# Performance work log

Hardware: AMD Instinct MI355X
Metric: run time of the kernel (lower is better)

## Reference

```python
import jax, jax.numpy as jnp
import numpy as np

D_MODEL, D_STATE, EXPAND, D_CONV = 96, 16, 2, 3
D_INNER = EXPAND * D_MODEL  # 192
DT_RANK = -(-D_MODEL // 16)  # 6
K = 4
B, H, W = 4, 64, 64


def setup_inputs() -> dict:
    key = jax.random.key(0)
    ks = jax.random.split(key, 12)
    x = jax.random.normal(ks[0], (B, H, W, D_MODEL), jnp.float32)
    in_proj_w = jax.random.normal(ks[1], (2 * D_INNER, D_MODEL), jnp.float32) * 0.02
    conv_w = jax.random.normal(ks[2], (D_INNER, 1, D_CONV, D_CONV), jnp.float32) * 0.1
    conv_b = jnp.zeros((D_INNER,), jnp.float32)
    x_proj_w = jax.random.normal(ks[3], (K, DT_RANK + 2 * D_STATE, D_INNER), jnp.float32) * 0.02
    dt_proj_w = jax.random.uniform(ks[4], (K, D_INNER, DT_RANK), jnp.float32,
                                   -DT_RANK ** -0.5, DT_RANK ** -0.5)
    dt = jnp.exp(jax.random.uniform(ks[5], (K, D_INNER)) *
                 (np.log(0.1) - np.log(0.001)) + np.log(0.001))
    dt = jnp.clip(dt, 1e-4, None)
    dt_proj_b = dt + jnp.log(-jnp.expm1(-dt))  # inverse-softplus init
    A_logs = jnp.tile(jnp.log(jnp.arange(1, D_STATE + 1, dtype=jnp.float32))[None, :],
                      (K * D_INNER, 1))
    Ds = jnp.ones((K * D_INNER,), jnp.float32)
    norm_g = jnp.ones((D_INNER,), jnp.float32)
    norm_b = jnp.zeros((D_INNER,), jnp.float32)
    out_proj_w = jax.random.normal(ks[6], (D_MODEL, D_INNER), jnp.float32) * 0.02
    return dict(x=x, in_proj_w=in_proj_w, conv_w=conv_w, conv_b=conv_b,
                x_proj_w=x_proj_w, dt_proj_w=dt_proj_w, dt_proj_b=dt_proj_b,
                A_logs=A_logs, Ds=Ds, norm_g=norm_g, norm_b=norm_b,
                out_proj_w=out_proj_w)


def _selective_scan(u, delta, A, Bmat, Cmat, Dvec):
    # u,delta: (B,K,D,L)  A: (K,D,N)  Bmat,Cmat: (B,K,N,L)  Dvec: (K,D)
    uT = jnp.moveaxis(u, -1, 0)      # (L,B,K,D)
    dT = jnp.moveaxis(delta, -1, 0)  # (L,B,K,D)
    BT = jnp.moveaxis(Bmat, -1, 0)   # (L,B,K,N)
    CT = jnp.moveaxis(Cmat, -1, 0)   # (L,B,K,N)
    h0 = jnp.zeros(u.shape[:3] + (A.shape[-1],), u.dtype)  # (B,K,D,N)

    def step(h, inp):
        u_t, d_t, B_t, C_t = inp
        dA = jnp.exp(d_t[..., None] * A)                       # (B,K,D,N)
        dBu = (d_t * u_t)[..., None] * B_t[..., None, :]       # (B,K,D,N)
        h = dA * h + dBu
        y = jnp.sum(h * C_t[..., None, :], axis=-1)            # (B,K,D)
        return h, y

    _, ys = jax.lax.scan(step, h0, (uT, dT, BT, CT))
    y = jnp.moveaxis(ys, 0, -1)  # (B,K,D,L)
    return y + Dvec[None, :, :, None] * u


def reference(x, in_proj_w, conv_w, conv_b, x_proj_w, dt_proj_w, dt_proj_b,
              A_logs, Ds, norm_g, norm_b, out_proj_w):
    Bn, Hn, Wn, _ = x.shape
    L = Hn * Wn
    xz = x @ in_proj_w.T                       # (B,H,W,2*Dinner)
    xi, z = jnp.split(xz, 2, axis=-1)
    xi = jnp.transpose(xi, (0, 3, 1, 2))       # (B,Dinner,H,W)
    xi = jax.lax.conv_general_dilated(xi, conv_w, (1, 1), 'SAME',
                                      feature_group_count=D_INNER,
                                      dimension_numbers=('NCHW', 'OIHW', 'NCHW'))
    xi = xi + conv_b[None, :, None, None]
    xi = jax.nn.silu(xi)

    # 4 scan directions
    x_hw = xi.reshape(Bn, D_INNER, L)
    x_wh = jnp.transpose(xi, (0, 1, 3, 2)).reshape(Bn, D_INNER, L)
    x_hwwh = jnp.stack([x_hw, x_wh], axis=1)               # (B,2,D,L)
    xs = jnp.concatenate([x_hwwh, jnp.flip(x_hwwh, axis=-1)], axis=1)  # (B,4,D,L)

    x_dbl = jnp.einsum('bkdl,kcd->bkcl', xs, x_proj_w)
    dts, Bs, Cs = jnp.split(x_dbl, [DT_RANK, DT_RANK + D_STATE], axis=2)
    dts = jnp.einsum('bkrl,kdr->bkdl', dts, dt_proj_w)
    delta = jax.nn.softplus(dts + dt_proj_b[None, :, :, None])

    A = -jnp.exp(A_logs).reshape(K, D_INNER, D_STATE)
    Dv = Ds.reshape(K, D_INNER)
    out_y = _selective_scan(xs, delta, A, Bs, Cs, Dv)       # (B,4,D,L)

    inv_y = jnp.flip(out_y[:, 2:4], axis=-1)                # (B,2,D,L)
    wh_y = jnp.transpose(out_y[:, 1].reshape(Bn, D_INNER, Wn, Hn),
                         (0, 1, 3, 2)).reshape(Bn, D_INNER, L)
    invwh_y = jnp.transpose(inv_y[:, 1].reshape(Bn, D_INNER, Wn, Hn),
                            (0, 1, 3, 2)).reshape(Bn, D_INNER, L)
    y = out_y[:, 0] + inv_y[:, 0] + wh_y + invwh_y          # (B,D,L)

    y = jnp.transpose(y, (0, 2, 1)).reshape(Bn, Hn, Wn, D_INNER)
    mu = jnp.mean(y, axis=-1, keepdims=True)
    var = jnp.var(y, axis=-1, keepdims=True)
    y = (y - mu) * jax.lax.rsqrt(var + 1e-5) * norm_g + norm_b
    y = y * jax.nn.silu(z)
    return y @ out_proj_w.T
```

## Files before the change

kernel.cpp:

```cpp
#include <hip/hip_runtime.h>
#include <math.h>

#define BN 4
#define LL 4096
#define DM 96
#define DI 192
#define NS 16
#define KK 4
#define RR 6
#define NCH 64
#define LC (LL/NCH)
#define BCW 40

__device__ __forceinline__ float silu_f(float x){ return x / (1.f + __expf(-x)); }
__device__ __forceinline__ float softplus_f(float x){
  return fmaxf(x, 0.f) + __logf(1.f + __expf(-fabsf(x)));
}
__device__ __forceinline__ void fma4(float4& a, const float4 w, const float4 v){
  a.x = fmaf(w.x, v.x, a.x); a.y = fmaf(w.y, v.y, a.y);
  a.z = fmaf(w.z, v.z, a.z); a.w = fmaf(w.w, v.w, a.w);
}

__global__ __launch_bounds__(256) void k1_inproj(const float* __restrict__ x,
    const float* __restrict__ w, float* __restrict__ xi, float* __restrict__ zs)
{
  __shared__ float xt[16][DM];
  __shared__ float wt[64][DM+4];
  int blk = blockIdx.x;
  int b = blk >> 8;
  int l0 = (blk & 255) << 4;
  int tid = threadIdx.x;
  for (int idx = tid; idx < 16*24; idx += 256) {
    int t = idx / 24, jj = idx % 24;
    ((float4*)xt[t])[jj] = *(const float4*)(x + ((size_t)(b*LL + l0 + t))*DM + 4*jj);
  }
  int cl = tid & 63;
  int tb = (tid >> 6) * 4;
  for (int ct = 0; ct < 6; ++ct) {
    int c0 = ct*64;
    __syncthreads();
    for (int idx = tid; idx < 64*24; idx += 256) {
      int r = idx / 24, jj = idx % 24;
      ((float4*)wt[r])[jj] = *(const float4*)(w + (size_t)(c0 + r)*DM + 4*jj);
    }
    __syncthreads();
    float4 a0={0,0,0,0}, a1={0,0,0,0}, a2={0,0,0,0}, a3={0,0,0,0};
    const float4* wr = (const float4*)wt[cl];
    const float4* x0 = (const float4*)xt[tb+0];
    const float4* x1 = (const float4*)xt[tb+1];
    const float4* x2 = (const float4*)xt[tb+2];
    const float4* x3 = (const float4*)xt[tb+3];
    #pragma unroll
    for (int jj = 0; jj < 24; ++jj) {
      float4 w4 = wr[jj];
      fma4(a0, w4, x0[jj]); fma4(a1, w4, x1[jj]);
      fma4(a2, w4, x2[jj]); fma4(a3, w4, x3[jj]);
    }
    float accs[4] = { (a0.x+a0.y)+(a0.z+a0.w), (a1.x+a1.y)+(a1.z+a1.w),
                      (a2.x+a2.y)+(a2.z+a2.w), (a3.x+a3.y)+(a3.z+a3.w) };
    int c = c0 + cl;
    #pragma unroll
    for (int tt = 0; tt < 4; ++tt) {
      int l = l0 + tb + tt;
      float v = accs[tt];
      if (c < DI) xi[((size_t)(b*LL + l))*DI + c] = v;
      else        zs[((size_t)(b*LL + l))*DI + (c - DI)] = silu_f(v);
    }
  }
}

__global__ __launch_bounds__(256) void k2_conv(const float* __restrict__ xi,
    const float* __restrict__ cw, const float* __restrict__ cb,
    float* __restrict__ U0, float* __restrict__ U1)
{
  int n = blockIdx.x*256 + threadIdx.x;
  if (n >= BN*LL*48) return;
  int c4 = n % 48;
  int w_ = (n / 48) & 63;
  int h_ = (n / (48*64)) & 63;
  int b  = n / (48*LL);
  int c  = c4 * 4;
  float4 acc = { cb[c], cb[c+1], cb[c+2], cb[c+3] };
  #pragma unroll
  for (int kh = 0; kh < 3; ++kh) {
    int hh = h_ + kh - 1;
    if (hh < 0 || hh >= 64) continue;
    #pragma unroll
    for (int kw = 0; kw < 3; ++kw) {
      int ww2 = w_ + kw - 1;
      if (ww2 < 0 || ww2 >= 64) continue;
      float4 v = *(const float4*)(xi + ((size_t)(b*LL) + hh*64 + ww2)*DI + c);
      int tap = kh*3 + kw;
      acc.x = fmaf(v.x, cw[(c+0)*9 + tap], acc.x);
      acc.y = fmaf(v.y, cw[(c+1)*9 + tap], acc.y);
      acc.z = fmaf(v.z, cw[(c+2)*9 + tap], acc.z);
      acc.w = fmaf(v.w, cw[(c+3)*9 + tap], acc.w);
    }
  }
  float4 o = { silu_f(acc.x), silu_f(acc.y), silu_f(acc.z), silu_f(acc.w) };
  *(float4*)(U0 + ((size_t)(b*LL) + h_*64 + w_)*DI + c) = o;
  *(float4*)(U1 + ((size_t)(b*LL) + w_*64 + h_)*DI + c) = o;
}

__global__ __launch_bounds__(320) void k3_xproj(const float* __restrict__ U0,
    const float* __restrict__ U1, const float* __restrict__ xw,
    float* __restrict__ BC)
{
  __shared__ float  ut[32][DI];
  __shared__ float4 wT[48][41];
  __shared__ float  cS[32][BCW];
  int blk = blockIdx.x;
  int tile = blk & 127; int k = (blk >> 7) & 3; int b = blk >> 9;
  int l0 = tile << 5;
  int tid = threadIdx.x;
  const float* U = (k & 1) ? U1 : U0;
  int b4k = b*KK + k;
  for (int idx = tid; idx < 32*48; idx += 320) {
    int r = idx / 48, jj = idx % 48;
    ((float4*)ut[r])[jj] = *(const float4*)(U + ((size_t)(b*LL + l0 + r))*DI + 4*jj);
  }
  for (int idx = tid; idx < 38*48; idx += 320) {
    int cc = idx / 48, jj = idx % 48;
    wT[jj][cc] = *(const float4*)(xw + (size_t)(k*38 + cc)*DI + 4*jj);
  }
  __syncthreads();
  int cc = tid % 40;
  int rg = tid / 40;
  if (cc < 38) {
    float4 a0={0,0,0,0}, a1={0,0,0,0}, a2={0,0,0,0}, a3={0,0,0,0};
    const float4* u0 = (const float4*)ut[rg*4+0];
    const float4* u1 = (const float4*)ut[rg*4+1];
    const float4* u2 = (const float4*)ut[rg*4+2];
    const float4* u3 = (const float4*)ut[rg*4+3];
    #pragma unroll
    for (int jj = 0; jj < 48; ++jj) {
      float4 w4 = wT[jj][cc];
      fma4(a0, w4, u0[jj]); fma4(a1, w4, u1[jj]);
      fma4(a2, w4, u2[jj]); fma4(a3, w4, u3[jj]);
    }
    int cp = (cc < RR) ? (32 + cc) : (cc - RR);
    cS[rg*4+0][cp] = (a0.x+a0.y)+(a0.z+a0.w);
    cS[rg*4+1][cp] = (a1.x+a1.y)+(a1.z+a1.w);
    cS[rg*4+2][cp] = (a2.x+a2.y)+(a2.z+a2.w);
    cS[rg*4+3][cp] = (a3.x+a3.y)+(a3.z+a3.w);
  } else {
    cS[rg*4+0][cc] = 0.f; cS[rg*4+1][cc] = 0.f;
    cS[rg*4+2][cc] = 0.f; cS[rg*4+3][cc] = 0.f;
  }
  __syncthreads();
  {
    int r = tid / 10, q = tid % 10;
    *(float4*)(BC + ((size_t)b4k*LL + l0 + r)*BCW + 4*q) = ((float4*)cS[r])[q];
  }
}

__device__ __forceinline__ void pow_tree(float e1, float* ep){
  ep[0]=e1;
  ep[1]=e1*e1;
  ep[2]=ep[1]*e1;  ep[3]=ep[1]*ep[1];
  ep[4]=ep[3]*e1;  ep[5]=ep[3]*ep[1]; ep[6]=ep[3]*ep[2]; ep[7]=ep[3]*ep[3];
  #pragma unroll
  for (int i=0;i<8;++i) ep[8+i]=ep[7]*ep[i];
}

__device__ __forceinline__ float delta_of(const float* __restrict__ row,
    const float* __restrict__ dw, float dtb1){
  float4 t4 = *(const float4*)(row + 32);
  float2 t2 = *(const float2*)(row + 36);
  float a = dtb1;
  a = fmaf(t4.x, dw[0], a); a = fmaf(t4.y, dw[1], a);
  a = fmaf(t4.z, dw[2], a); a = fmaf(t4.w, dw[3], a);
  a = fmaf(t2.x, dw[4], a); a = fmaf(t2.y, dw[5], a);
  return softplus_f(a);
}

__global__ __launch_bounds__(192) void k4a_pass1(const float* __restrict__ U0,
    const float* __restrict__ U1, const float* __restrict__ BC,
    const float* __restrict__ A_logs, const float* __restrict__ dtw,
    const float* __restrict__ dtb,
    float* __restrict__ hst, float* __restrict__ Ssum)
{
  int blk = blockIdx.x;
  int c = blk % NCH; int k = (blk / NCH) & 3; int b = blk / (NCH*4);
  int d = threadIdx.x;
  const float* U = (k & 1) ? U1 : U0;
  int b4k = b*KK + k;
  float an[NS];
  #pragma unroll
  for (int n = 0; n < NS; ++n) an[n] = -__expf(A_logs[(k*DI + d)*NS + n]);
  float a0 = an[0];
  bool chain = true;
  #pragma unroll
  for (int n = 1; n < NS; ++n)
    chain = chain && (fabsf(an[n] - a0*(float)(n+1)) <= 1e-3f*(float)(n+1));
  float dw[RR];
  #pragma unroll
  for (int r = 0; r < RR; ++r) dw[r] = dtw[(k*DI + d)*RR + r];
  float dtb1 = dtb[k*DI + d];
  float h[NS];
  #pragma unroll
  for (int n = 0; n < NS; ++n) h[n] = 0.f;
  float sd = 0.f;
  bool fwd = (k < 2);
  int lo = c * LC;
  int dir = fwd ? 1 : -1;
  int l = fwd ? lo : (lo + LC - 1);
  const float* pu = U + ((size_t)(b*LL) + l)*DI + d;
  const float* pbc = BC + ((size_t)b4k*LL + l)*BCW;
  intptr_t pinc = (intptr_t)dir * DI;
  intptr_t bcinc = (intptr_t)dir * BCW;
  #pragma unroll 2
  for (int s = 0; s < LC; ++s) {
    float dv = delta_of(pbc, dw, dtb1);
    float u  = *pu;
    float du = dv * u;
    sd += dv;
    const float4* b4p = (const float4*)pbc;
    float4 B0 = b4p[0], B1 = b4p[1], B2 = b4p[2], B3 = b4p[3];
    float Bv[NS] = {B0.x,B0.y,B0.z,B0.w, B1.x,B1.y,B1.z,B1.w,
                    B2.x,B2.y,B2.z,B2.w, B3.x,B3.y,B3.z,B3.w};
    if (chain) {
      float ep[NS];
      pow_tree(__expf(a0 * dv), ep);
      #pragma unroll
      for (int n = 0; n < NS; ++n) h[n] = fmaf(ep[n], h[n], du*Bv[n]);
    } else {
      #pragma unroll
      for (int n = 0; n < NS; ++n) h[n] = fmaf(__expf(an[n]*dv), h[n], du*Bv[n]);
    }
    pu += pinc; pbc += bcinc;
  }
  size_t base = ((size_t)b4k*NCH + c)*DI + d;
  float4* he = (float4*)(hst + base*NS);
  he[0] = make_float4(h[0], h[1], h[2], h[3]);
  he[1] = make_float4(h[4], h[5], h[6], h[7]);
  he[2] = make_float4(h[8], h[9], h[10],h[11]);
  he[3] = make_float4(h[12],h[13],h[14],h[15]);
  Ssum[base] = sd;
}

__global__ __launch_bounds__(256) void k4b_combine(float* __restrict__ hst,
    const float* __restrict__ Ssum, const float* __restrict__ A_logs)
{
  int blk = blockIdx.x;
  int dgrp = blk % 12; int k = (blk/12) & 3; int b = blk/48;
  int tid = threadIdx.x;
  int d = dgrp*16 + (tid >> 4);
  int n = tid & 15;
  int b4k = b*KK + k;
  float an = -__expf(A_logs[(k*DI + d)*NS + n]);
  bool fwd = (k < 2);
  float h = 0.f;
  for (int s = 0; s < NCH; ++s) {
    int c = fwd ? s : (NCH - 1 - s);
    size_t base = ((size_t)b4k*NCH + c)*DI + d;
    float he = hst[base*NS + n];
    hst[base*NS + n] = h;
    h = __expf(an * Ssum[base]) * h + he;
  }
}

__global__ __launch_bounds__(192) void k4c_pass2(const float* __restrict__ U0,
    const float* __restrict__ U1, const float* __restrict__ BC,
    const float* __restrict__ A_logs, const float* __restrict__ dtw,
    const float* __restrict__ dtb, const float* __restrict__ Dsv,
    const float* __restrict__ hst, float* __restrict__ ytot)
{
  int blk = blockIdx.x;
  int c = blk % NCH; int k = (blk / NCH) & 3; int b = blk / (NCH*4);
  int d = threadIdx.x;
  const float* U = (k & 1) ? U1 : U0;
  int b4k = b*KK + k;
  float an[NS];
  #pragma unroll
  for (int n = 0; n < NS; ++n) an[n] = -__expf(A_logs[(k*DI + d)*NS + n]);
  float a0 = an[0];
  bool chain = true;
  #pragma unroll
  for (int n = 1; n < NS; ++n)
    chain = chain && (fabsf(an[n] - a0*(float)(n+1)) <= 1e-3f*(float)(n+1));
  float dw[RR];
  #pragma unroll
  for (int r = 0; r < RR; ++r) dw[r] = dtw[(k*DI + d)*RR + r];
  float dtb1 = dtb[k*DI + d];
  float Dd = Dsv[k*DI + d];
  size_t base = ((size_t)b4k*NCH + c)*DI + d;
  float h[NS];
  {
    const float4* hi = (const float4*)(hst + base*NS);
    float4 h0 = hi[0], h1 = hi[1], h2 = hi[2], h3 = hi[3];
    h[0]=h0.x; h[1]=h0.y; h[2]=h0.z; h[3]=h0.w;
    h[4]=h1.x; h[5]=h1.y; h[6]=h1.z; h[7]=h1.w;
    h[8]=h2.x; h[9]=h2.y; h[10]=h2.z; h[11]=h2.w;
    h[12]=h3.x; h[13]=h3.y; h[14]=h3.z; h[15]=h3.w;
  }
  bool fwd = (k < 2);
  int lo = c * LC;
  int dir = fwd ? 1 : -1;
  int l = fwd ? lo : (lo + LC - 1);
  const float* pu = U + ((size_t)(b*LL) + l)*DI + d;
  const float* pbc = BC + ((size_t)b4k*LL + l)*BCW;
  intptr_t pinc = (intptr_t)dir * DI;
  intptr_t bcinc = (intptr_t)dir * BCW;
  bool odd = (k & 1);
  #pragma unroll 2
  for (int s = 0; s < LC; ++s) {
    float dv = delta_of(pbc, dw, dtb1);
    float u  = *pu;
    float du = dv * u;
    const float4* b4p = (const float4*)pbc;
    float4 B0 = b4p[0], B1 = b4p[1], B2 = b4p[2], B3 = b4p[3];
    float4 C0 = b4p[4], C1 = b4p[5], C2 = b4p[6], C3 = b4p[7];
    float Bv[NS] = {B0.x,B0.y,B0.z,B0.w, B1.x,B1.y,B1.z,B1.w,
                    B2.x,B2.y,B2.z,B2.w, B3.x,B3.y,B3.z,B3.w};
    float Cv[NS] = {C0.x,C0.y,C0.z,C0.w, C1.x,C1.y,C1.z,C1.w,
                    C2.x,C2.y,C2.z,C2.w, C3.x,C3.y,C3.z,C3.w};
    if (chain) {
      float ep[NS];
      pow_tree(__expf(a0 * dv), ep);
      #pragma unroll
      for (int n = 0; n < NS; ++n) h[n] = fmaf(ep[n], h[n], du*Bv[n]);
    } else {
      #pragma unroll
      for (int n = 0; n < NS; ++n) h[n] = fmaf(__expf(an[n]*dv), h[n], du*Bv[n]);
    }
    float p0 = Dd*u, p1 = 0.f, p2 = 0.f, p3 = 0.f;
    #pragma unroll
    for (int n = 0; n < NS; n += 4) {
      p0 = fmaf(h[n+0], Cv[n+0], p0);
      p1 = fmaf(h[n+1], Cv[n+1], p1);
      p2 = fmaf(h[n+2], Cv[n+2], p2);
      p3 = fmaf(h[n+3], Cv[n+3], p3);
    }
    int pos = odd ? (((l & 63) << 6) | (l >> 6)) : l;
    unsafeAtomicAdd(&ytot[((size_t)(b*LL) + pos)*DI + d], (p0+p1)+(p2+p3));
    l += dir; pu += pinc; pbc += bcinc;
  }
}

__global__ __launch_bounds__(384) void k5_final(const float* __restrict__ ytot,
    const float* __restrict__ zs, const float* __restrict__ g,
    const float* __restrict__ bb, const float* __restrict__ ow,
    float* __restrict__ out)
{
  __shared__ float yt[32][DI+4];
  __shared__ float muS[32], rsS[32];
  int blk = blockIdx.x;
  int b = blk >> 7; int l0 = (blk & 127) << 5;
  int tid = threadIdx.x;
  for (int idx = tid; idx < 32*48; idx += 384) {
    int r = idx / 48, jj = idx % 48;
    ((float4*)yt[r])[jj] = *(const float4*)(ytot + ((size_t)(b*LL) + l0 + r)*DI + 4*jj);
  }
  __syncthreads();
  if (tid < 256) {
    int r = tid >> 3, q = tid & 7;
    const float* row = yt[r];
    float s1 = 0.f, s2 = 0.f;
    #pragma unroll
    for (int i = 0; i < 24; ++i) {
      float v = row[q*24 + i];
      s1 += v; s2 += v*v;
    }
    s1 += __shfl_xor(s1, 1); s2 += __shfl_xor(s2, 1);
    s1 += __shfl_xor(s1, 2); s2 += __shfl_xor(s2, 2);
    s1 += __shfl_xor(s1, 4); s2 += __shfl_xor(s2, 4);
    if (q == 0) {
      float mu = s1 / (float)DI;
      float var = s2 / (float)DI - mu*mu;
      muS[r] = mu;
      rsS[r] = rsqrtf(var + 1e-5f);
    }
  }
  __syncthreads();
  for (int idx = tid; idx < 32*48; idx += 384) {
    int r = idx / 48, jj = idx % 48;
    float4 y = ((float4*)yt[r])[jj];
    float mu = muS[r], rs = rsS[r];
    float4 g4 = *(const float4*)(g + 4*jj);
    float4 b4 = *(const float4*)(bb + 4*jj);
    float4 z4 = *(const float4*)(zs + ((size_t)(b*LL) + l0 + r)*DI + 4*jj);
    float4 v;
    v.x = fmaf((y.x-mu)*rs, g4.x, b4.x) * z4.x;
    v.y = fmaf((y.y-mu)*rs, g4.y, b4.y) * z4.y;
    v.z = fmaf((y.z-mu)*rs, g4.z, b4.z) * z4.z;
    v.w = fmaf((y.w-mu)*rs, g4.w, b4.w) * z4.w;
    ((float4*)yt[r])[jj] = v;
  }
  __syncthreads();
  {
    int c = tid % 96;
    int rg = tid / 96;
    const float4* wrow = (const float4*)(ow + (size_t)c*DI);
    float4 acc[8];
    #pragma unroll
    for (int rr = 0; rr < 8; ++rr) acc[rr] = make_float4(0.f,0.f,0.f,0.f);
    #pragma unroll
    for (int ch = 0; ch < 6; ++ch) {
      float4 wreg[8];
      #pragma unroll
      for (int jj = 0; jj < 8; ++jj) wreg[jj] = wrow[ch*8 + jj];
      #pragma unroll
      for (int rr = 0; rr < 8; ++rr) {
        const float4* yr = (const float4*)yt[rg*8 + rr];
        #pragma unroll
        for (int jj = 0; jj < 8; ++jj) fma4(acc[rr], wreg[jj], yr[ch*8 + jj]);
      }
    }
    #pragma unroll
    for (int rr = 0; rr < 8; ++rr) {
      float v = (acc[rr].x+acc[rr].y)+(acc[rr].z+acc[rr].w);
      out[((size_t)(b*LL) + l0 + rg*8 + rr)*DM + c] = v;
    }
  }
}

extern "C" void kernel_launch(void* const* d_in, const int* in_sizes, int n_in,
                              void* d_out, int out_size, void* d_ws, size_t ws_size,
                              hipStream_t stream)
{
  const float* x    = (const float*)d_in[0];
  const float* ipw  = (const float*)d_in[1];
  const float* cw   = (const float*)d_in[2];
  const float* cb   = (const float*)d_in[3];
  const float* xpw  = (const float*)d_in[4];
  const float* dtwp = (const float*)d_in[5];
  const float* dtbp = (const float*)d_in[6];
  const float* alog = (const float*)d_in[7];
  const float* dsp  = (const float*)d_in[8];
  const float* ng   = (const float*)d_in[9];
  const float* nbp  = (const float*)d_in[10];
  const float* owp  = (const float*)d_in[11];
  float* out = (float*)d_out;

  float* ws = (float*)d_ws;
  size_t off = 0;
  float* ytot = ws + off; off += (size_t)BN*LL*DI;
  float* zs   = ws + off; off += (size_t)BN*LL*DI;
  float* xi   = ws + off; off += (size_t)BN*LL*DI;
  float* U0   = ws + off; off += (size_t)BN*LL*DI;
  float* U1   = ws + off; off += (size_t)BN*LL*DI;
  float* BC   = ws + off; off += (size_t)BN*KK*LL*BCW;
  float* hst  = ws + off; off += (size_t)BN*KK*NCH*DI*NS;
  float* Ssum = ws + off; off += (size_t)BN*KK*NCH*DI;
  (void)ws_size; (void)in_sizes; (void)n_in; (void)out_size;

  hipMemsetAsync(ytot, 0, (size_t)BN*LL*DI*sizeof(float), stream);
  k1_inproj<<<dim3(BN*256), dim3(256), 0, stream>>>(x, ipw, xi, zs);
  k2_conv<<<dim3((BN*LL*48 + 255)/256), dim3(256), 0, stream>>>(xi, cw, cb, U0, U1);
  k3_xproj<<<dim3(BN*KK*128), dim3(320), 0, stream>>>(U0, U1, xpw, BC);
  k4a_pass1<<<dim3(BN*KK*NCH), dim3(192), 0, stream>>>(U0, U1, BC, alog, dtwp, dtbp, hst, Ssum);
  k4b_combine<<<dim3(BN*KK*12), dim3(256), 0, stream>>>(hst, Ssum, alog);
  k4c_pass2<<<dim3(BN*KK*NCH), dim3(192), 0, stream>>>(U0, U1, BC, alog, dtwp, dtbp, dsp, hst, ytot);
  k5_final<<<dim3(BN*128), dim3(384), 0, stream>>>(ytot, zs, ng, nbp, owp, out);
}
```

Baseline: 388.6 us.

## Restructure in-projection so each thread owns one output channel across 16 tokens

```diff
diff --git a/kernel.cpp b/kernel.cpp
--- a/kernel.cpp
+++ b/kernel.cpp
@@ -21,50 +21,40 @@
   a.z = fmaf(w.z, v.z, a.z); a.w = fmaf(w.w, v.w, a.w);
 }
 
-__global__ __launch_bounds__(256) void k1_inproj(const float* __restrict__ x,
+__global__ __launch_bounds__(384) void k1_inproj(const float* __restrict__ x,
     const float* __restrict__ w, float* __restrict__ xi, float* __restrict__ zs)
 {
   __shared__ float xt[16][DM];
-  __shared__ float wt[64][DM+4];
   int blk = blockIdx.x;
   int b = blk >> 8;
   int l0 = (blk & 255) << 4;
   int tid = threadIdx.x;
-  for (int idx = tid; idx < 16*24; idx += 256) {
-    int t = idx / 24, jj = idx % 24;
+  {
+    int t = tid / 24, jj = tid % 24;
     ((float4*)xt[t])[jj] = *(const float4*)(x + ((size_t)(b*LL + l0 + t))*DM + 4*jj);
   }
-  int cl = tid & 63;
-  int tb = (tid >> 6) * 4;
-  for (int ct = 0; ct < 6; ++ct) {
-    int c0 = ct*64;
-    __syncthreads();
-    for (int idx = tid; idx < 64*24; idx += 256) {
-      int r = idx / 24, jj = idx % 24;
-      ((float4*)wt[r])[jj] = *(const float4*)(w + (size_t)(c0 + r)*DM + 4*jj);
-    }
-    __syncthreads();
-    float4 a0={0,0,0,0}, a1={0,0,0,0}, a2={0,0,0,0}, a3={0,0,0,0};
-    const float4* wr = (const float4*)wt[cl];
-    const float4* x0 = (const float4*)xt[tb+0];
-    const float4* x1 = (const float4*)xt[tb+1];
-    const float4* x2 = (const float4*)xt[tb+2];
-    const float4* x3 = (const float4*)xt[tb+3];
-    #pragma unroll
-    for (int jj = 0; jj < 24; ++jj) {
-      float4 w4 = wr[jj];
-      fma4(a0, w4, x0[jj]); fma4(a1, w4, x1[jj]);
-      fma4(a2, w4, x2[jj]); fma4(a3, w4, x3[jj]);
-    }
-    float accs[4] = { (a0.x+a0.y)+(a0.z+a0.w), (a1.x+a1.y)+(a1.z+a1.w),
-                      (a2.x+a2.y)+(a2.z+a2.w), (a3.x+a3.y)+(a3.z+a3.w) };
-    int c = c0 + cl;
-    #pragma unroll
-    for (int tt = 0; tt < 4; ++tt) {
-      int l = l0 + tb + tt;
-      float v = accs[tt];
-      if (c < DI) xi[((size_t)(b*LL + l))*DI + c] = v;
-      else        zs[((size_t)(b*LL + l))*DI + (c - DI)] = silu_f(v);
+  __syncthreads();
+  const float4* wrow = (const float4*)(w + (size_t)tid*DM);
+  float4 acc[16];
+  #pragma unroll
+  for (int r = 0; r < 16; ++r) acc[r] = make_float4(0.f,0.f,0.f,0.f);
+  #pragma unroll 4
+  for (int jj = 0; jj < 24; ++jj) {
+    float4 w4 = wrow[jj];
+    #pragma unroll
+    for (int r = 0; r < 16; ++r) fma4(acc[r], w4, ((const float4*)xt[r])[jj]);
+  }
+  if (tid < DI) {
+    #pragma unroll
+    for (int r = 0; r < 16; ++r) {
+      float v = (acc[r].x+acc[r].y)+(acc[r].z+acc[r].w);
+      xi[((size_t)(b*LL + l0 + r))*DI + tid] = v;
+    }
+  } else {
+    #pragma unroll
+    for (int r = 0; r < 16; ++r) {
+      float v = (acc[r].x+acc[r].y)+(acc[r].z+acc[r].w);
+      zs[((size_t)(b*LL + l0 + r))*DI + (tid - DI)] = silu_f(v);
     }
   }
 }
@@ -446,7 +436,7 @@
   (void)ws_size; (void)in_sizes; (void)n_in; (void)out_size;
 
   hipMemsetAsync(ytot, 0, (size_t)BN*LL*DI*sizeof(float), stream);
-  k1_inproj<<<dim3(BN*256), dim3(256), 0, stream>>>(x, ipw, xi, zs);
+  k1_inproj<<<dim3(BN*256), dim3(384), 0, stream>>>(x, ipw, xi, zs);
   k2_conv<<<dim3((BN*LL*48 + 255)/256), dim3(256), 0, stream>>>(xi, cw, cb, U0, U1);
   k3_xproj<<<dim3(BN*KK*128), dim3(320), 0, stream>>>(U0, U1, xpw, BC);
   k4a_pass1<<<dim3(BN*KK*NCH), dim3(192), 0, stream>>>(U0, U1, BC, alog, dtwp, dtbp, hst, Ssum);
```

New measurement: 337.5 us. 1.15x faster.
